# Performance work log

Measured on AMD Instinct MI355X. Metric: run time of the kernel, lower is better.

## Reference

```python
import jax, jax.numpy as jnp
import numpy as np

B, S, T, D = 8, 8, 256, 256          # batch, series, time_steps, input_dim
H, DK = 8, 64                         # attn_heads, attn_dim
HD = H * DK                           # 512
L = 2                                 # attn_layers
F = 256                               # mlp_dim
R = 512                               # resolution
M = 128                               # number of mid-points sampled this step
EPS = 1e-5


def setup_inputs() -> dict:
    key = jax.random.key(0)
    ks = iter(jax.random.split(key, 64))

    def rn(shape, scale=0.05):
        return scale * jax.random.normal(next(ks), shape, dtype=jnp.float32)

    inp = {
        'encoded': jax.random.normal(next(ks), (B, S, T, D), dtype=jnp.float32),
        'true_u': jax.random.uniform(next(ks), (B, S, T), dtype=jnp.float32),
        'mid_idx': jnp.sort(jax.random.randint(next(ks), (M,), 0, T)),
        'left_idx': jax.random.randint(next(ks), (M,), 0, T),
        'right_idx': jax.random.randint(next(ks), (M,), 0, T),
        'i': 3,
        # dimension_shift
        'ds_W': rn((D, HD)), 'ds_b': jnp.zeros((HD,), jnp.float32),
        # per-layer, per-head key-creator MLPs (stacked): (D+1) -> F -> F -> DK
        'kW1': rn((L, H, D + 1, F)), 'kb1': jnp.zeros((L, H, F), jnp.float32),
        'kW2': rn((L, H, F, F)),     'kb2': jnp.zeros((L, H, F), jnp.float32),
        'kW3': rn((L, H, F, DK)),    'kb3': jnp.zeros((L, H, DK), jnp.float32),
        # value-creator MLPs
        'vW1': rn((L, H, D + 1, F)), 'vb1': jnp.zeros((L, H, F), jnp.float32),
        'vW2': rn((L, H, F, F)),     'vb2': jnp.zeros((L, H, F), jnp.float32),
        'vW3': rn((L, H, F, DK)),    'vb3': jnp.zeros((L, H, DK), jnp.float32),
        # attention / feed-forward layer norms
        'ln1_g': jnp.ones((L, HD), jnp.float32), 'ln1_b': jnp.zeros((L, HD), jnp.float32),
        'ln2_g': jnp.ones((L, HD), jnp.float32), 'ln2_b': jnp.zeros((L, HD), jnp.float32),
        # feed-forwards
        'ffW1': rn((L, HD, HD)), 'ffb1': jnp.zeros((L, HD), jnp.float32),
        'ffW2': rn((L, HD, HD)), 'ffb2': jnp.zeros((L, HD), jnp.float32),
        # dist_extractors MLP: HD -> F -> F -> R
        'deW1': rn((HD, F)), 'deb1': jnp.zeros((F,), jnp.float32),
        'deW2': rn((F, F)),  'deb2': jnp.zeros((F,), jnp.float32),
        'deW3': rn((F, R)),  'deb3': jnp.zeros((R,), jnp.float32),
    }
    return inp


def _mlp_heads(x, W1, b1, W2, b2, W3, b3):
    # x: [B,S,T,D+1]; weights: [L,H,...] -> out [L,B,S,T,H,DK]
    h = jax.nn.relu(jnp.einsum('bstc,lhcf->lbsthf', x, W1) + b1[:, None, None, None])
    h = jax.nn.relu(jnp.einsum('lbsthf,lhfg->lbsthg', h, W2) + b2[:, None, None, None])
    return jnp.einsum('lbsthg,lhgd->lbsthd', h, W3) + b3[:, None, None, None]


def _ln(x, g, b):
    mu = jnp.mean(x, axis=-1, keepdims=True)
    var = jnp.mean(jnp.square(x - mu), axis=-1, keepdims=True)
    return (x - mu) * jax.lax.rsqrt(var + EPS) * g + b


def reference(encoded, true_u, mid_idx, left_idx, right_idx, i,
              ds_W, ds_b,
              kW1, kb1, kW2, kb2, kW3, kb3,
              vW1, vb1, vW2, vb2, vW3, vb3,
              ln1_g, ln1_b, ln2_g, ln2_b,
              ffW1, ffb1, ffW2, ffb2,
              deW1, deb1, deW2, deb2, deW3, deb3):
    # merged_input = cat([encoded, true_u[..., None]])  -> [B,S,T,D+1]
    merged = jnp.concatenate([encoded, true_u[..., None]], axis=-1)

    keys = _mlp_heads(merged, kW1, kb1, kW2, kb2, kW3, kb3)   # [L,B,S,T,H,DK]
    values = _mlp_heads(merged, vW1, vb1, vW2, vb2, vW3, vb3)  # [L,B,S,T,H,DK]

    srange = jnp.arange(S)
    # n=1 neighbor: time index = loop counter m for series < i, else right[m]
    # (faithful to keys_hist[:, :i, mid:mid+1] in the original)
    idx1 = jnp.where(srange[None, :] < i, jnp.arange(M)[:, None], right_idx[:, None])  # [M,S]

    def gather_neighbors(kv):  # kv: [L,B,S,T,H,DK] -> [L,B,M,S,2,H,DK]
        n0 = jnp.transpose(kv[:, :, :, left_idx], (0, 1, 3, 2, 4, 5))  # [L,B,M,S,H,DK]
        n1 = kv[:, :, srange[None, :], idx1]                            # [L,B,M,S,H,DK]
        return jnp.stack([n0, n1], axis=4)

    nk = gather_neighbors(keys)
    nv = gather_neighbors(values)

    pred = encoded[:, i, mid_idx]                  # [B,M,D]
    att_value = pred @ ds_W + ds_b                 # [B,M,HD]

    scale = DK ** (-0.5)
    for l in range(L):
        avh = att_value.reshape(B, M, H, DK)
        prod = jnp.einsum('bmhd,bmsnhd->bmhsn', avh, nk[l]) * scale
        w = jax.nn.softmax(prod, axis=-1)          # softmax over n only, as in source
        att = jnp.einsum('bmhsn,bmsnhd->bmhd', w, nv[l]).reshape(B, M, HD)
        x = _ln(att_value + att, ln1_g[l], ln1_b[l])
        ff = jax.nn.relu(x @ ffW1[l] + ffb1[l]) @ ffW2[l] + ffb2[l]
        att_value = _ln(x + ff, ln2_g[l], ln2_b[l])

    h = jax.nn.relu(att_value @ deW1 + deb1)
    h = jax.nn.relu(h @ deW2 + deb2)
    logits = h @ deW3 + deb3                       # [B,M,R]
    return logits
```

## Files before the change

kernel.cpp:

```cpp
#include <hip/hip_runtime.h>
#include <hip/hip_bf16.h>

#define NB 8
#define NS 8
#define NT 256
#define ND 256
#define NH 8
#define NDK 64
#define NHD 512
#define NL 2
#define NF 256
#define NR 512
#define NM 128
#define NTOK 16384
#define NROW 1024

typedef __attribute__((ext_vector_type(8))) short short8;
typedef __attribute__((ext_vector_type(4))) float f32x4;

__device__ __forceinline__ unsigned short f2bf(float x) {
    unsigned u = __builtin_bit_cast(unsigned, x);
    unsigned r = (u + 0x7fffu + ((u >> 16) & 1u)) >> 16;
    return (unsigned short)r;
}
__device__ __forceinline__ float bf2f(unsigned short x) {
    return __builtin_bit_cast(float, ((unsigned)x) << 16);
}
__device__ __forceinline__ float wred(float v) {
#pragma unroll
    for (int o = 32; o > 0; o >>= 1) v += __shfl_xor(v, o, 64);
    return v;
}

__global__ __launch_bounds__(256) void prep_all(
    const float* __restrict__ enc,
    const float* __restrict__ kW1, const float* __restrict__ kW2, const float* __restrict__ kW3,
    const float* __restrict__ vW1, const float* __restrict__ vW2, const float* __restrict__ vW3,
    const float* __restrict__ dsW, const float* __restrict__ ffW1,
    const float* __restrict__ ffW2, const float* __restrict__ deW1,
    const float* __restrict__ deW2, const float* __restrict__ deW3,
    unsigned short* __restrict__ XF, unsigned short* __restrict__ WP,
    float* __restrict__ W1L, unsigned short* __restrict__ WG) {
    __shared__ float T[32][257];
    int bid = blockIdx.x, tid = threadIdx.x;
    if (bid < 512) {
        int t0 = bid * 32;
        const float* src = enc + (size_t)t0 * 256;
#pragma unroll
        for (int it = 0; it < 8; ++it) {
            int f4 = it * 256 + tid;
            int row = f4 >> 6, c = (f4 & 63) * 4;
            float4 v = *(const float4*)(src + row * 256 + c);
            T[row][c] = v.x; T[row][c + 1] = v.y; T[row][c + 2] = v.z; T[row][c + 3] = v.w;
        }
        __syncthreads();
        int tile = t0 >> 7, g = (t0 >> 6) & 1, nt0 = (t0 >> 4) & 3;
#pragma unroll
        for (int i = 0; i < 32; i += 8) {
            int o = tid * 32 + i;
            int lane = (o >> 3) & 63, ntp = (o >> 9) & 1, kc = o >> 10;
            int id = lane & 15, quad = lane >> 4;
            __align__(16) unsigned short p[8];
#pragma unroll
            for (int j = 0; j < 8; ++j) p[j] = f2bf(T[ntp * 16 + id][kc * 32 + quad * 8 + j]);
            size_t dsto = ((size_t)((((tile * 8 + kc) * 2 + g) * 4 + (nt0 + ntp)) * 64 + lane)) * 8;
            *(uint4*)(XF + dsto) = *(uint4*)p;
        }
    } else if (bid < 1280) {
        int lb = bid - 512;
        int combo = lb / 24, r = lb % 24;
        int st = r >> 3, kc = r & 7;
        int kvv = combo >> 4, l = (combo >> 3) & 1, h = combo & 7;
        unsigned short* dstc = WP + (size_t)combo * 147456;
        if (st < 2) {
            const float* W = (st == 0) ? (kvv ? vW1 : kW1) : (kvv ? vW2 : kW2);
            int rows = (st == 0) ? 257 : 256;
            const float* src = W + ((size_t)(l * 8 + h) * rows + kc * 32) * 256;
#pragma unroll
            for (int it = 0; it < 8; ++it) {
                int f4 = it * 256 + tid;
                int row = f4 >> 6, c = (f4 & 63) * 4;
                float4 v = *(const float4*)(src + (size_t)row * 256 + c);
                T[row][c] = v.x; T[row][c + 1] = v.y; T[row][c + 2] = v.z; T[row][c + 3] = v.w;
            }
            __syncthreads();
            unsigned short* dst = dstc + st * 65536 + kc * 8192;
#pragma unroll
            for (int i = 0; i < 32; i += 8) {
                int o = tid * 32 + i;
                int lane = (o >> 3) & 63, ftile = o >> 9;
                int id = lane & 15, quad = lane >> 4;
                __align__(16) unsigned short p[8];
#pragma unroll
                for (int j = 0; j < 8; ++j) p[j] = f2bf(T[quad * 8 + j][ftile * 16 + id]);
                *(uint4*)(dst + o) = *(uint4*)p;
            }
            if (st == 0 && kc == 0) {
                const float* hw = (kvv ? vW1 : kW1) + (size_t)(l * 8 + h) * 257 * 256;
                W1L[combo * 256 + tid] = hw[65536 + tid];
            }
        } else {
            const float* src = (kvv ? vW3 : kW3) + ((size_t)(l * 8 + h) * 256 + kc * 32) * 64;
#pragma unroll
            for (int it = 0; it < 2; ++it) {
                int f4 = it * 256 + tid;
                int row = f4 >> 4, c = (f4 & 15) * 4;
                float4 v = *(const float4*)(src + (size_t)row * 64 + c);
                T[row][c] = v.x; T[row][c + 1] = v.y; T[row][c + 2] = v.z; T[row][c + 3] = v.w;
            }
            __syncthreads();
            unsigned short* dst = dstc + 131072 + kc * 2048;
            int o = tid * 8;
            int lane = tid & 63, ftile = tid >> 6;
            int id = lane & 15, quad = lane >> 4;
            __align__(16) unsigned short p[8];
#pragma unroll
            for (int j = 0; j < 8; ++j) p[j] = f2bf(T[quad * 8 + j][ftile * 16 + id]);
            *(uint4*)(dst + o) = *(uint4*)p;
        }
    } else {
        int lb0 = bid - 1280;
        const float* src; int N, kc, ng; size_t base;
        if (lb0 < 32)       { int lb = lb0;       src = dsW;           N = 512; base = 0;       kc = lb >> 2; ng = lb & 3; }
        else if (lb0 < 96)  { int lb = lb0 - 32;  src = ffW1;          N = 512; base = 131072;  kc = lb >> 2; ng = lb & 3; }
        else if (lb0 < 160) { int lb = lb0 - 96;  src = ffW1 + 262144; N = 512; base = 393216;  kc = lb >> 2; ng = lb & 3; }
        else if (lb0 < 224) { int lb = lb0 - 160; src = ffW2;          N = 512; base = 655360;  kc = lb >> 2; ng = lb & 3; }
        else if (lb0 < 288) { int lb = lb0 - 224; src = ffW2 + 262144; N = 512; base = 917504;  kc = lb >> 2; ng = lb & 3; }
        else if (lb0 < 320) { int lb = lb0 - 288; src = deW1;          N = 256; base = 1179648; kc = lb >> 1; ng = lb & 1; }
        else if (lb0 < 336) { int lb = lb0 - 320; src = deW2;          N = 256; base = 1310720; kc = lb >> 1; ng = lb & 1; }
        else                { int lb = lb0 - 336; src = deW3;          N = 512; base = 1376256; kc = lb >> 2; ng = lb & 3; }
        int NTl = N >> 4;
        const float* s = src + (size_t)(kc * 32) * N + ng * 128;
#pragma unroll
        for (int it = 0; it < 4; ++it) {
            int f4 = it * 256 + tid;
            int row = f4 >> 5, c = (f4 & 31) * 4;
            float4 v = *(const float4*)(s + (size_t)row * N + c);
            T[row][c] = v.x; T[row][c + 1] = v.y; T[row][c + 2] = v.z; T[row][c + 3] = v.w;
        }
        __syncthreads();
        unsigned short* d = WG + base + (size_t)(kc * NTl + ng * 8) * 512;
#pragma unroll
        for (int i = 0; i < 16; i += 8) {
            int o = tid * 16 + i;
            int lane = (o >> 3) & 63, ntl = o >> 9;
            int id = lane & 15, quad = lane >> 4;
            __align__(16) unsigned short p[8];
#pragma unroll
            for (int j = 0; j < 8; ++j) p[j] = f2bf(T[quad * 8 + j][ntl * 16 + id]);
            *(uint4*)(d + o) = *(uint4*)p;
        }
    }
}

__global__ __launch_bounds__(256, 4) void heads_mlp(
    const float* __restrict__ tu, const unsigned short* __restrict__ XF,
    const unsigned short* __restrict__ WP, const float* __restrict__ W1L,
    const float* __restrict__ kb1, const float* __restrict__ kb2, const float* __restrict__ kb3,
    const float* __restrict__ vb1, const float* __restrict__ vb2, const float* __restrict__ vb3,
    unsigned short* __restrict__ KV) {
    __shared__ __align__(16) unsigned short smem[16896];

    const int tid = threadIdx.x;
    const int w2 = tid >> 6, lane = tid & 63, id = lane & 15, quad = lane >> 4;
    const int combo = blockIdx.x & 31, t64 = blockIdx.x >> 5;
    const int kvv = combo >> 4, l = (combo >> 3) & 1, h = combo & 7;
    const int r0 = t64 * 64;
    const int tile128 = t64 >> 1, g = t64 & 1;
    const unsigned short* WF1 = WP + (size_t)combo * 147456;
    const unsigned short* WF2 = WF1 + 65536;
    const unsigned short* WF3 = WF1 + 131072;
    const float* b1 = (kvv ? vb1 : kb1) + (l * 8 + h) * 256;
    const float* b2 = (kvv ? vb2 : kb2) + (l * 8 + h) * 256;
    const float* b3 = (kvv ? vb3 : kb3) + (l * 8 + h) * 64;

    short8 afb[2][4];
#pragma unroll
    for (int ft = 0; ft < 4; ++ft) {
        afb[0][ft] = *(const short8*)(WF1 + (size_t)((w2 * 4 + ft) * 64 + lane) * 8);
        afb[1][ft] = *(const short8*)(WF1 + (size_t)((16 + w2 * 4 + ft) * 64 + lane) * 8);
    }
    {
        const uint4* s = (const uint4*)(XF + (size_t)tile128 * 32768 + g * 2048);
        uint4* d = (uint4*)smem;
#pragma unroll
        for (int kc = 0; kc < 8; ++kc) d[kc * 256 + tid] = s[kc * 512 + tid];
    }
    __syncthreads();

    f32x4 acc[4][4];
#pragma unroll
    for (int i = 0; i < 4; ++i)
#pragma unroll
        for (int j = 0; j < 4; ++j) acc[i][j] = (f32x4){0.f, 0.f, 0.f, 0.f};

    {
#pragma unroll
        for (int kc = 0; kc < 8; ++kc) {
            short8 tn[4];
            if (kc + 2 < 8) {
#pragma unroll
                for (int ft = 0; ft < 4; ++ft)
                    tn[ft] = *(const short8*)(WF1 + (size_t)(((kc + 2) * 16 + w2 * 4 + ft) * 64 + lane) * 8);
            }
            short8 bf[4];
#pragma unroll
            for (int nt = 0; nt < 4; ++nt)
                bf[nt] = *(const short8*)(smem + (size_t)(kc * 4 + nt) * 512 + lane * 8);
#pragma unroll
            for (int ft = 0; ft < 4; ++ft)
#pragma unroll
                for (int nt = 0; nt < 4; ++nt)
                    acc[ft][nt] = __builtin_amdgcn_mfma_f32_16x16x32_bf16(afb[kc & 1][ft], bf[nt], acc[ft][nt], 0, 0, 0);
            if (kc + 2 < 8) {
#pragma unroll
                for (int ft = 0; ft < 4; ++ft) afb[kc & 1][ft] = tn[ft];
            }
        }
    }
    __syncthreads();
    {
        float ur[4];
#pragma unroll
        for (int nt = 0; nt < 4; ++nt) ur[nt] = tu[r0 + nt * 16 + id];
#pragma unroll
        for (int ft = 0; ft < 4; ++ft) {
            int fb = w2 * 64 + ft * 16 + quad * 4;
            float4 bb = *(const float4*)(b1 + fb);
            float4 wl = *(const float4*)(W1L + combo * 256 + fb);
            const float* bbp = (const float*)&bb;
            const float* wlp = (const float*)&wl;
#pragma unroll
            for (int nt = 0; nt < 4; ++nt) {
                unsigned short p[4];
#pragma unroll
                for (int r = 0; r < 4; ++r) {
                    float v = acc[ft][nt][r] + bbp[r] + ur[nt] * wlp[r];
                    p[r] = f2bf(fmaxf(v, 0.f));
                }
                uint2 pk;
                pk.x = (unsigned)p[0] | ((unsigned)p[1] << 16);
                pk.y = (unsigned)p[2] | ((unsigned)p[3] << 16);
                *(uint2*)(smem + (size_t)(nt * 16 + id) * 264 + fb) = pk;
            }
        }
    }
    __syncthreads();

#pragma unroll
    for (int i = 0; i < 4; ++i)
#pragma unroll
        for (int j = 0; j < 4; ++j) acc[i][j] = (f32x4){0.f, 0.f, 0.f, 0.f};
    {
#pragma unroll
        for (int ft = 0; ft < 4; ++ft) {
            afb[0][ft] = *(const short8*)(WF2 + (size_t)((w2 * 4 + ft) * 64 + lane) * 8);
            afb[1][ft] = *(const short8*)(WF2 + (size_t)((16 + w2 * 4 + ft) * 64 + lane) * 8);
        }
#pragma unroll
        for (int kc = 0; kc < 8; ++kc) {
            short8 tn[4];
            if (kc + 2 < 8) {
#pragma unroll
                for (int ft = 0; ft < 4; ++ft)
                    tn[ft] = *(const short8*)(WF2 + (size_t)(((kc + 2) * 16 + w2 * 4 + ft) * 64 + lane) * 8);
            }
            short8 bf[4];
#pragma unroll
            for (int nt = 0; nt < 4; ++nt)
                bf[nt] = *(const short8*)(smem + (size_t)(nt * 16 + id) * 264 + kc * 32 + quad * 8);
#pragma unroll
            for (int ft = 0; ft < 4; ++ft)
#pragma unroll
                for (int nt = 0; nt < 4; ++nt)
                    acc[ft][nt] = __builtin_amdgcn_mfma_f32_16x16x32_bf16(afb[kc & 1][ft], bf[nt], acc[ft][nt], 0, 0, 0);
            if (kc + 2 < 8) {
#pragma unroll
                for (int ft = 0; ft < 4; ++ft) afb[kc & 1][ft] = tn[ft];
            }
        }
    }
    __syncthreads();
#pragma unroll
    for (int ft = 0; ft < 4; ++ft) {
        int fb = w2 * 64 + ft * 16 + quad * 4;
        float4 bb = *(const float4*)(b2 + fb);
        const float* bbp = (const float*)&bb;
#pragma unroll
        for (int nt = 0; nt < 4; ++nt) {
            unsigned short p[4];
#pragma unroll
            for (int r = 0; r < 4; ++r)
                p[r] = f2bf(fmaxf(acc[ft][nt][r] + bbp[r], 0.f));
            uint2 pk;
            pk.x = (unsigned)p[0] | ((unsigned)p[1] << 16);
            pk.y = (unsigned)p[2] | ((unsigned)p[3] << 16);
            *(uint2*)(smem + (size_t)(nt * 16 + id) * 264 + fb) = pk;
        }
    }
    __syncthreads();

    f32x4 a3[4];
#pragma unroll
    for (int i = 0; i < 4; ++i) a3[i] = (f32x4){0.f, 0.f, 0.f, 0.f};
    {
        short8 af3[4], af3n[4];
#pragma unroll
        for (int ft = 0; ft < 4; ++ft)
            af3[ft] = *(const short8*)(WF3 + (size_t)(ft * 64 + lane) * 8);
#pragma unroll
        for (int kc = 0; kc < 8; ++kc) {
            if (kc < 7) {
#pragma unroll
                for (int ft = 0; ft < 4; ++ft)
                    af3n[ft] = *(const short8*)(WF3 + (size_t)(((kc + 1) * 4 + ft) * 64 + lane) * 8);
            }
            short8 b3f = *(const short8*)(smem + (size_t)(w2 * 16 + id) * 264 + kc * 32 + quad * 8);
#pragma unroll
            for (int ft = 0; ft < 4; ++ft)
                a3[ft] = __builtin_amdgcn_mfma_f32_16x16x32_bf16(af3[ft], b3f, a3[ft], 0, 0, 0);
#pragma unroll
            for (int ft = 0; ft < 4; ++ft) af3[ft] = af3n[ft];
        }
    }
    __syncthreads();
    {
        int tl = w2 * 16 + id;
#pragma unroll
        for (int ft = 0; ft < 4; ++ft) {
            int dk0 = ft * 16 + quad * 4;
            float4 bb = *(const float4*)(b3 + dk0);
            const float* bbp = (const float*)&bb;
            unsigned short p[4];
#pragma unroll
            for (int r = 0; r < 4; ++r) p[r] = f2bf(a3[ft][r] + bbp[r]);
            uint2 pk;
            pk.x = (unsigned)p[0] | ((unsigned)p[1] << 16);
            pk.y = (unsigned)p[2] | ((unsigned)p[3] << 16);
            *(uint2*)(smem + (size_t)tl * 72 + dk0) = pk;
        }
    }
    __syncthreads();
    {
#pragma unroll
        for (int it = 0; it < 2; ++it) {
            int tl = it * 32 + (tid >> 3), part = tid & 7;
            uint4 v = *(const uint4*)(smem + (size_t)tl * 72 + part * 8);
            size_t base = ((size_t)combo << 20) + (size_t)(r0 + tl) * 64 + part * 8;
            *(uint4*)(KV + base) = v;
        }
    }
}

__global__ __launch_bounds__(256) void gemm_ds(
    const float* __restrict__ enc, const int* __restrict__ mid,
    const int* __restrict__ ip, const unsigned short* __restrict__ WF,
    const float* __restrict__ bias, float* __restrict__ outf) {
    int tid = threadIdx.x, wv = tid >> 6, lane = tid & 63;
    int id = lane & 15, quad = lane >> 4;
    int ntile = blockIdx.x * 4 + wv;
    int n0 = ntile * 16, m0 = blockIdx.y * 32;
    int iv = ip[0];
    int r0 = m0 + id, r1 = m0 + 16 + id;
    const float* a0p = enc + (((size_t)((r0 >> 7) * 8 + iv)) * 256 + mid[r0 & 127]) * 256 + quad * 8;
    const float* a1p = enc + (((size_t)((r1 >> 7) * 8 + iv)) * 256 + mid[r1 & 127]) * 256 + quad * 8;
    f32x4 acc[2];
    acc[0] = (f32x4){0.f, 0.f, 0.f, 0.f};
    acc[1] = (f32x4){0.f, 0.f, 0.f, 0.f};
#pragma unroll
    for (int kc = 0; kc < 8; ++kc) {
        short8 bw = *(const short8*)(WF + (size_t)((kc * 32 + ntile) * 64 + lane) * 8);
        float4 u0 = *(const float4*)(a0p + kc * 32);
        float4 u1 = *(const float4*)(a0p + kc * 32 + 4);
        float4 w0 = *(const float4*)(a1p + kc * 32);
        float4 w1 = *(const float4*)(a1p + kc * 32 + 4);
        short8 a0, a1;
        a0[0] = (short)f2bf(u0.x); a0[1] = (short)f2bf(u0.y); a0[2] = (short)f2bf(u0.z); a0[3] = (short)f2bf(u0.w);
        a0[4] = (short)f2bf(u1.x); a0[5] = (short)f2bf(u1.y); a0[6] = (short)f2bf(u1.z); a0[7] = (short)f2bf(u1.w);
        a1[0] = (short)f2bf(w0.x); a1[1] = (short)f2bf(w0.y); a1[2] = (short)f2bf(w0.z); a1[3] = (short)f2bf(w0.w);
        a1[4] = (short)f2bf(w1.x); a1[5] = (short)f2bf(w1.y); a1[6] = (short)f2bf(w1.z); a1[7] = (short)f2bf(w1.w);
        acc[0] = __builtin_amdgcn_mfma_f32_16x16x32_bf16(a0, bw, acc[0], 0, 0, 0);
        acc[1] = __builtin_amdgcn_mfma_f32_16x16x32_bf16(a1, bw, acc[1], 0, 0, 0);
    }
    float bv = bias[n0 + id];
#pragma unroll
    for (int mt = 0; mt < 2; ++mt) {
#pragma unroll
        for (int r = 0; r < 4; ++r) {
            int row = m0 + mt * 16 + quad * 4 + r;
            outf[(size_t)row * 512 + n0 + id] = acc[mt][r] + bv;
        }
    }
}

__global__ __launch_bounds__(256) void gemm_bf16(
    const unsigned short* __restrict__ A, const unsigned short* __restrict__ WF,
    const float* __restrict__ bias, const float* __restrict__ res,
    float* __restrict__ outf, unsigned short* __restrict__ outb,
    int K, int N, int relu) {
    int tid = threadIdx.x, wv = tid >> 6, lane = tid & 63;
    int id = lane & 15, quad = lane >> 4;
    int ntile = blockIdx.x * 4 + wv;
    int n0 = ntile * 16, m0 = blockIdx.y * 32;
    int NTl = N >> 4, KC = K >> 5;
    f32x4 acc[2];
    acc[0] = (f32x4){0.f, 0.f, 0.f, 0.f};
    acc[1] = (f32x4){0.f, 0.f, 0.f, 0.f};
    short8 bw = *(const short8*)(WF + (size_t)(ntile * 64 + lane) * 8);
    short8 a0 = *(const short8*)(A + (size_t)(m0 + id) * K + quad * 8);
    short8 a1 = *(const short8*)(A + (size_t)(m0 + 16 + id) * K + quad * 8);
    for (int kc = 0; kc < KC; ++kc) {
        short8 bwn, a0n, a1n;
        if (kc + 1 < KC) {
            bwn = *(const short8*)(WF + (size_t)(((kc + 1) * NTl + ntile) * 64 + lane) * 8);
            a0n = *(const short8*)(A + (size_t)(m0 + id) * K + (kc + 1) * 32 + quad * 8);
            a1n = *(const short8*)(A + (size_t)(m0 + 16 + id) * K + (kc + 1) * 32 + quad * 8);
        }
        acc[0] = __builtin_amdgcn_mfma_f32_16x16x32_bf16(a0, bw, acc[0], 0, 0, 0);
        acc[1] = __builtin_amdgcn_mfma_f32_16x16x32_bf16(a1, bw, acc[1], 0, 0, 0);
        bw = bwn; a0 = a0n; a1 = a1n;
    }
    float bv = bias[n0 + id];
#pragma unroll
    for (int mt = 0; mt < 2; ++mt) {
#pragma unroll
        for (int r = 0; r < 4; ++r) {
            int row = m0 + mt * 16 + quad * 4 + r;
            int n = n0 + id;
            float v = acc[mt][r] + bv;
            if (res) v += res[(size_t)row * N + n];
            if (relu) v = fmaxf(v, 0.f);
            if (outf) outf[(size_t)row * N + n] = v;
            if (outb) outb[(size_t)row * N + n] = f2bf(v);
        }
    }
}

__global__ __launch_bounds__(256) void attn_ln(
    const float* __restrict__ attv, const unsigned short* __restrict__ KV,
    const int* __restrict__ left, const int* __restrict__ right,
    const int* __restrict__ ip,
    const float* __restrict__ g, const float* __restrict__ bb,
    float* __restrict__ xout, unsigned short* __restrict__ xoutb, int l) {
    int tid = threadIdx.x, wv = tid >> 6, lane = tid & 63;
    int gid = blockIdx.x * 4 + wv;
    int b = gid >> 7, m = gid & 127;
    int iv = ip[0];
    int lt = left[m], rt = right[m];
    int h = lane >> 3, d8 = lane & 7;
    const unsigned short* kb = KV + ((size_t)(l * 8 + h) << 20);
    const unsigned short* vb = KV + ((size_t)(16 + l * 8 + h) << 20);
    float av8[8], att8[8];
    {
        const float* avp = attv + (size_t)gid * 512 + lane * 8;
        float4 u0 = *(const float4*)(avp);
        float4 u1 = *(const float4*)(avp + 4);
        av8[0] = u0.x; av8[1] = u0.y; av8[2] = u0.z; av8[3] = u0.w;
        av8[4] = u1.x; av8[5] = u1.y; av8[6] = u1.z; av8[7] = u1.w;
    }
#pragma unroll
    for (int j = 0; j < 8; ++j) att8[j] = 0.f;
#pragma unroll 2
    for (int s = 0; s < 8; ++s) {
        int t1 = (s < iv) ? m : rt;
        size_t o0 = (size_t)((b * 8 + s) * 256 + lt) * 64 + d8 * 8;
        size_t o1 = (size_t)((b * 8 + s) * 256 + t1) * 64 + d8 * 8;
        uint4 k0u = *(const uint4*)(kb + o0);
        uint4 k1u = *(const uint4*)(kb + o1);
        uint4 v0u = *(const uint4*)(vb + o0);
        uint4 v1u = *(const uint4*)(vb + o1);
        const unsigned short* k0 = (const unsigned short*)&k0u;
        const unsigned short* k1 = (const unsigned short*)&k1u;
        const unsigned short* v0 = (const unsigned short*)&v0u;
        const unsigned short* v1 = (const unsigned short*)&v1u;
        float p0 = 0.f, p1 = 0.f;
#pragma unroll
        for (int j = 0; j < 8; ++j) {
            p0 += av8[j] * bf2f(k0[j]);
            p1 += av8[j] * bf2f(k1[j]);
        }
#pragma unroll
        for (int o = 1; o < 8; o <<= 1) {
            p0 += __shfl_xor(p0, o, 64);
            p1 += __shfl_xor(p1, o, 64);
        }
        p0 *= 0.125f; p1 *= 0.125f;
        float mx = fmaxf(p0, p1);
        float e0 = __expf(p0 - mx), e1 = __expf(p1 - mx);
        float inv = 1.f / (e0 + e1);
        float w0 = e0 * inv, w1 = e1 * inv;
#pragma unroll
        for (int j = 0; j < 8; ++j)
            att8[j] += w0 * bf2f(v0[j]) + w1 * bf2f(v1[j]);
    }
    float x8[8], sum = 0.f;
#pragma unroll
    for (int j = 0; j < 8; ++j) { x8[j] = av8[j] + att8[j]; sum += x8[j]; }
    float mu = wred(sum) * (1.f / 512.f);
    float s2 = 0.f;
#pragma unroll
    for (int j = 0; j < 8; ++j) { float d = x8[j] - mu; s2 += d * d; }
    float rs = rsqrtf(wred(s2) * (1.f / 512.f) + 1e-5f);
    {
        const float* gp = g + lane * 8;
        const float* bp = bb + lane * 8;
        float* of = xout + (size_t)gid * 512 + lane * 8;
        unsigned short* ob = xoutb + (size_t)gid * 512 + lane * 8;
        __align__(16) float vout[8];
        __align__(16) unsigned short pb[8];
#pragma unroll
        for (int j = 0; j < 8; ++j) {
            float v = (x8[j] - mu) * rs * gp[j] + bp[j];
            vout[j] = v; pb[j] = f2bf(v);
        }
        *(float4*)(of) = *(float4*)vout;
        *(float4*)(of + 4) = *(float4*)(vout + 4);
        *(uint4*)(ob) = *(uint4*)pb;
    }
}

__global__ __launch_bounds__(256) void ln_k(const float* __restrict__ in,
                                            const float* __restrict__ g,
                                            const float* __restrict__ bb,
                                            float* __restrict__ out,
                                            unsigned short* __restrict__ outb) {
    int tid = threadIdx.x, wv = tid >> 6, lane = tid & 63;
    int gid = blockIdx.x * 4 + wv;
    float x8[8], sum = 0.f;
    {
        const float* ip = in + (size_t)gid * 512 + lane * 8;
        float4 u0 = *(const float4*)(ip);
        float4 u1 = *(const float4*)(ip + 4);
        x8[0] = u0.x; x8[1] = u0.y; x8[2] = u0.z; x8[3] = u0.w;
        x8[4] = u1.x; x8[5] = u1.y; x8[6] = u1.z; x8[7] = u1.w;
    }
#pragma unroll
    for (int j = 0; j < 8; ++j) sum += x8[j];
    float mu = wred(sum) * (1.f / 512.f);
    float s2 = 0.f;
#pragma unroll
    for (int j = 0; j < 8; ++j) { float d = x8[j] - mu; s2 += d * d; }
    float rs = rsqrtf(wred(s2) * (1.f / 512.f) + 1e-5f);
    {
        const float* gp = g + lane * 8;
        const float* bp = bb + lane * 8;
        float* of = out + (size_t)gid * 512 + lane * 8;
        unsigned short* ob = outb + (size_t)gid * 512 + lane * 8;
        __align__(16) float vout[8];
        __align__(16) unsigned short pb[8];
#pragma unroll
        for (int j = 0; j < 8; ++j) {
            float v = (x8[j] - mu) * rs * gp[j] + bp[j];
            vout[j] = v; pb[j] = f2bf(v);
        }
        *(float4*)(of) = *(float4*)vout;
        *(float4*)(of + 4) = *(float4*)(vout + 4);
        *(uint4*)(ob) = *(uint4*)pb;
    }
}

extern "C" void kernel_launch(void* const* d_in, const int* in_sizes, int n_in,
                              void* d_out, int out_size, void* d_ws, size_t ws_size,
                              hipStream_t stream) {
    const float* encoded = (const float*)d_in[0];
    const float* true_u  = (const float*)d_in[1];
    const int* mid_idx   = (const int*)d_in[2];
    const int* left_idx  = (const int*)d_in[3];
    const int* right_idx = (const int*)d_in[4];
    const int* ip        = (const int*)d_in[5];
    const float* ds_W = (const float*)d_in[6];
    const float* ds_b = (const float*)d_in[7];
    const float* kW1 = (const float*)d_in[8];
    const float* kb1 = (const float*)d_in[9];
    const float* kW2 = (const float*)d_in[10];
    const float* kb2 = (const float*)d_in[11];
    const float* kW3 = (const float*)d_in[12];
    const float* kb3 = (const float*)d_in[13];
    const float* vW1 = (const float*)d_in[14];
    const float* vb1 = (const float*)d_in[15];
    const float* vW2 = (const float*)d_in[16];
    const float* vb2 = (const float*)d_in[17];
    const float* vW3 = (const float*)d_in[18];
    const float* vb3 = (const float*)d_in[19];
    const float* ln1_g = (const float*)d_in[20];
    const float* ln1_b = (const float*)d_in[21];
    const float* ln2_g = (const float*)d_in[22];
    const float* ln2_b = (const float*)d_in[23];
    const float* ffW1 = (const float*)d_in[24];
    const float* ffb1 = (const float*)d_in[25];
    const float* ffW2 = (const float*)d_in[26];
    const float* ffb2 = (const float*)d_in[27];
    const float* deW1 = (const float*)d_in[28];
    const float* deb1 = (const float*)d_in[29];
    const float* deW2 = (const float*)d_in[30];
    const float* deb2 = (const float*)d_in[31];
    const float* deW3 = (const float*)d_in[32];
    const float* deb3 = (const float*)d_in[33];

    char* ws = (char*)d_ws;
    unsigned short* XF    = (unsigned short*)(ws + 0);
    unsigned short* WP    = (unsigned short*)(ws + 8388608);
    float* W1L            = (float*)(ws + 17825792);
    unsigned short* KV    = (unsigned short*)(ws + 17858560);
    unsigned short* WG    = (unsigned short*)(ws + 84967424);
    float* ATTV           = (float*)(ws + 87982080);
    float* XBUF           = (float*)(ws + 90079232);
    float* YBUF           = (float*)(ws + 92176384);
    unsigned short* ATTVB = (unsigned short*)(ws + 94273536);
    unsigned short* XBUFB = (unsigned short*)(ws + 95322112);
    unsigned short* FBUFB = (unsigned short*)(ws + 96370688);
    unsigned short* DE1B = XBUFB;
    unsigned short* DE2B = FBUFB;

    unsigned short* WGds    = WG + 0;
    unsigned short* WGff1_0 = WG + 131072;
    unsigned short* WGff1_1 = WG + 393216;
    unsigned short* WGff2_0 = WG + 655360;
    unsigned short* WGff2_1 = WG + 917504;
    unsigned short* WGde1   = WG + 1179648;
    unsigned short* WGde2   = WG + 1310720;
    unsigned short* WGde3   = WG + 1376256;

    prep_all<<<1648, 256, 0, stream>>>(encoded, kW1, kW2, kW3, vW1, vW2, vW3,
                                       ds_W, ffW1, ffW2, deW1, deW2, deW3,
                                       XF, WP, W1L, WG);
    heads_mlp<<<8192, 256, 0, stream>>>(true_u, XF, WP, W1L, kb1, kb2, kb3,
                                        vb1, vb2, vb3, KV);
    gemm_ds<<<dim3(8, 32), 256, 0, stream>>>(encoded, mid_idx, ip, WGds, ds_b, ATTV);
    for (int l = 0; l < 2; ++l) {
        attn_ln<<<256, 256, 0, stream>>>(ATTV, KV, left_idx, right_idx, ip,
                                         ln1_g + l * 512, ln1_b + l * 512,
                                         XBUF, XBUFB, l);
        gemm_bf16<<<dim3(8, 32), 256, 0, stream>>>(XBUFB, (l ? WGff1_1 : WGff1_0),
                                                   ffb1 + l * 512, nullptr,
                                                   nullptr, FBUFB, 512, 512, 1);
        gemm_bf16<<<dim3(8, 32), 256, 0, stream>>>(FBUFB, (l ? WGff2_1 : WGff2_0),
                                                   ffb2 + l * 512, XBUF,
                                                   YBUF, nullptr, 512, 512, 0);
        ln_k<<<256, 256, 0, stream>>>(YBUF, ln2_g + l * 512, ln2_b + l * 512, ATTV, ATTVB);
    }
    gemm_bf16<<<dim3(4, 32), 256, 0, stream>>>(ATTVB, WGde1, deb1, nullptr,
                                               nullptr, DE1B, 512, 256, 1);
    gemm_bf16<<<dim3(4, 32), 256, 0, stream>>>(DE1B, WGde2, deb2, nullptr,
                                               nullptr, DE2B, 256, 256, 1);
    gemm_bf16<<<dim3(8, 32), 256, 0, stream>>>(DE2B, WGde3, deb3, nullptr,
                                               (float*)d_out, nullptr, 256, 512, 0);
}
```

Baseline: 440.1 us.

## Fuse tail kernels into one persistent kernel with atomic grid barriers

Replaces the chain of twelve small tail launches (ds projection, attention+LN, FF GEMMs, LN, distribution MLP) with one 256-block persistent kernel. Stages are separated by software grid barriers built on atomic counters, which are zeroed in prep_all. This removes per-launch overhead and the idle gaps between small kernels. The barriers assume all 256 blocks are resident at once and add spin-wait cost at each stage boundary.

Result: slower. 581.2 us (+32.1%).

```diff
diff --git a/kernel.cpp b/kernel.cpp
--- a/kernel.cpp
+++ b/kernel.cpp
@@ -32,6 +32,17 @@
     return v;
 }
 
+__device__ __forceinline__ void gridbar(unsigned* c) {
+    __syncthreads();
+    if (threadIdx.x == 0) {
+        __hip_atomic_fetch_add(c, 1u, __ATOMIC_RELEASE, __HIP_MEMORY_SCOPE_AGENT);
+        while (__hip_atomic_load(c, __ATOMIC_RELAXED, __HIP_MEMORY_SCOPE_AGENT) < 256u)
+            __builtin_amdgcn_s_sleep(16);
+        (void)__hip_atomic_load(c, __ATOMIC_ACQUIRE, __HIP_MEMORY_SCOPE_AGENT);
+    }
+    __syncthreads();
+}
+
 __global__ __launch_bounds__(256) void prep_all(
     const float* __restrict__ enc,
     const float* __restrict__ kW1, const float* __restrict__ kW2, const float* __restrict__ kW3,
@@ -40,9 +51,11 @@
     const float* __restrict__ ffW2, const float* __restrict__ deW1,
     const float* __restrict__ deW2, const float* __restrict__ deW3,
     unsigned short* __restrict__ XF, unsigned short* __restrict__ WP,
-    float* __restrict__ W1L, unsigned short* __restrict__ WG) {
+    float* __restrict__ W1L, unsigned short* __restrict__ WG,
+    unsigned* __restrict__ BAR) {
     __shared__ float T[32][257];
     int bid = blockIdx.x, tid = threadIdx.x;
+    if (bid == 0 && tid < 16) BAR[tid] = 0;
     if (bid < 512) {
         int t0 = bid * 32;
         const float* src = enc + (size_t)t0 * 256;
@@ -352,60 +365,18 @@
     }
 }
 
-__global__ __launch_bounds__(256) void gemm_ds(
-    const float* __restrict__ enc, const int* __restrict__ mid,
-    const int* __restrict__ ip, const unsigned short* __restrict__ WF,
-    const float* __restrict__ bias, float* __restrict__ outf) {
-    int tid = threadIdx.x, wv = tid >> 6, lane = tid & 63;
-    int id = lane & 15, quad = lane >> 4;
-    int ntile = blockIdx.x * 4 + wv;
-    int n0 = ntile * 16, m0 = blockIdx.y * 32;
-    int iv = ip[0];
-    int r0 = m0 + id, r1 = m0 + 16 + id;
-    const float* a0p = enc + (((size_t)((r0 >> 7) * 8 + iv)) * 256 + mid[r0 & 127]) * 256 + quad * 8;
-    const float* a1p = enc + (((size_t)((r1 >> 7) * 8 + iv)) * 256 + mid[r1 & 127]) * 256 + quad * 8;
-    f32x4 acc[2];
-    acc[0] = (f32x4){0.f, 0.f, 0.f, 0.f};
-    acc[1] = (f32x4){0.f, 0.f, 0.f, 0.f};
-#pragma unroll
-    for (int kc = 0; kc < 8; ++kc) {
-        short8 bw = *(const short8*)(WF + (size_t)((kc * 32 + ntile) * 64 + lane) * 8);
-        float4 u0 = *(const float4*)(a0p + kc * 32);
-        float4 u1 = *(const float4*)(a0p + kc * 32 + 4);
-        float4 w0 = *(const float4*)(a1p + kc * 32);
-        float4 w1 = *(const float4*)(a1p + kc * 32 + 4);
-        short8 a0, a1;
-        a0[0] = (short)f2bf(u0.x); a0[1] = (short)f2bf(u0.y); a0[2] = (short)f2bf(u0.z); a0[3] = (short)f2bf(u0.w);
-        a0[4] = (short)f2bf(u1.x); a0[5] = (short)f2bf(u1.y); a0[6] = (short)f2bf(u1.z); a0[7] = (short)f2bf(u1.w);
-        a1[0] = (short)f2bf(w0.x); a1[1] = (short)f2bf(w0.y); a1[2] = (short)f2bf(w0.z); a1[3] = (short)f2bf(w0.w);
-        a1[4] = (short)f2bf(w1.x); a1[5] = (short)f2bf(w1.y); a1[6] = (short)f2bf(w1.z); a1[7] = (short)f2bf(w1.w);
-        acc[0] = __builtin_amdgcn_mfma_f32_16x16x32_bf16(a0, bw, acc[0], 0, 0, 0);
-        acc[1] = __builtin_amdgcn_mfma_f32_16x16x32_bf16(a1, bw, acc[1], 0, 0, 0);
-    }
-    float bv = bias[n0 + id];
-#pragma unroll
-    for (int mt = 0; mt < 2; ++mt) {
-#pragma unroll
-        for (int r = 0; r < 4; ++r) {
-            int row = m0 + mt * 16 + quad * 4 + r;
-            outf[(size_t)row * 512 + n0 + id] = acc[mt][r] + bv;
-        }
-    }
-}
-
-__global__ __launch_bounds__(256) void gemm_bf16(
+__device__ __forceinline__ void gemm_stage(
     const unsigned short* __restrict__ A, const unsigned short* __restrict__ WF,
     const float* __restrict__ bias, const float* __restrict__ res,
     float* __restrict__ outf, unsigned short* __restrict__ outb,
-    int K, int N, int relu) {
+    int K, int N, int relu, int bx, int by) {
     int tid = threadIdx.x, wv = tid >> 6, lane = tid & 63;
     int id = lane & 15, quad = lane >> 4;
-    int ntile = blockIdx.x * 4 + wv;
-    int n0 = ntile * 16, m0 = blockIdx.y * 32;
+    int ntile = bx * 4 + wv;
+    int n0 = ntile * 16, m0 = by * 32;
     int NTl = N >> 4, KC = K >> 5;
-    f32x4 acc[2];
-    acc[0] = (f32x4){0.f, 0.f, 0.f, 0.f};
-    acc[1] = (f32x4){0.f, 0.f, 0.f, 0.f};
+    f32x4 acc0 = (f32x4){0.f, 0.f, 0.f, 0.f};
+    f32x4 acc1 = (f32x4){0.f, 0.f, 0.f, 0.f};
     short8 bw = *(const short8*)(WF + (size_t)(ntile * 64 + lane) * 8);
     short8 a0 = *(const short8*)(A + (size_t)(m0 + id) * K + quad * 8);
     short8 a1 = *(const short8*)(A + (size_t)(m0 + 16 + id) * K + quad * 8);
@@ -416,18 +387,19 @@
             a0n = *(const short8*)(A + (size_t)(m0 + id) * K + (kc + 1) * 32 + quad * 8);
             a1n = *(const short8*)(A + (size_t)(m0 + 16 + id) * K + (kc + 1) * 32 + quad * 8);
         }
-        acc[0] = __builtin_amdgcn_mfma_f32_16x16x32_bf16(a0, bw, acc[0], 0, 0, 0);
-        acc[1] = __builtin_amdgcn_mfma_f32_16x16x32_bf16(a1, bw, acc[1], 0, 0, 0);
+        acc0 = __builtin_amdgcn_mfma_f32_16x16x32_bf16(a0, bw, acc0, 0, 0, 0);
+        acc1 = __builtin_amdgcn_mfma_f32_16x16x32_bf16(a1, bw, acc1, 0, 0, 0);
         bw = bwn; a0 = a0n; a1 = a1n;
     }
     float bv = bias[n0 + id];
 #pragma unroll
     for (int mt = 0; mt < 2; ++mt) {
+        f32x4 av = mt ? acc1 : acc0;
 #pragma unroll
         for (int r = 0; r < 4; ++r) {
             int row = m0 + mt * 16 + quad * 4 + r;
             int n = n0 + id;
-            float v = acc[mt][r] + bv;
+            float v = av[r] + bv;
             if (res) v += res[(size_t)row * N + n];
             if (relu) v = fmaxf(v, 0.f);
             if (outf) outf[(size_t)row * N + n] = v;
@@ -436,127 +408,196 @@
     }
 }
 
-__global__ __launch_bounds__(256) void attn_ln(
-    const float* __restrict__ attv, const unsigned short* __restrict__ KV,
+__global__ __launch_bounds__(256) void tail_fused(
+    const float* __restrict__ enc, const int* __restrict__ mid,
     const int* __restrict__ left, const int* __restrict__ right,
     const int* __restrict__ ip,
-    const float* __restrict__ g, const float* __restrict__ bb,
-    float* __restrict__ xout, unsigned short* __restrict__ xoutb, int l) {
-    int tid = threadIdx.x, wv = tid >> 6, lane = tid & 63;
-    int gid = blockIdx.x * 4 + wv;
-    int b = gid >> 7, m = gid & 127;
-    int iv = ip[0];
-    int lt = left[m], rt = right[m];
-    int h = lane >> 3, d8 = lane & 7;
-    const unsigned short* kb = KV + ((size_t)(l * 8 + h) << 20);
-    const unsigned short* vb = KV + ((size_t)(16 + l * 8 + h) << 20);
-    float av8[8], att8[8];
-    {
-        const float* avp = attv + (size_t)gid * 512 + lane * 8;
-        float4 u0 = *(const float4*)(avp);
-        float4 u1 = *(const float4*)(avp + 4);
-        av8[0] = u0.x; av8[1] = u0.y; av8[2] = u0.z; av8[3] = u0.w;
-        av8[4] = u1.x; av8[5] = u1.y; av8[6] = u1.z; av8[7] = u1.w;
-    }
-#pragma unroll
-    for (int j = 0; j < 8; ++j) att8[j] = 0.f;
+    const unsigned short* __restrict__ KV, const unsigned short* __restrict__ WG,
+    const float* __restrict__ ds_b,
+    const float* __restrict__ ln1_g, const float* __restrict__ ln1_b,
+    const float* __restrict__ ln2_g, const float* __restrict__ ln2_b,
+    const float* __restrict__ ffb1, const float* __restrict__ ffb2,
+    const float* __restrict__ deb1, const float* __restrict__ deb2,
+    const float* __restrict__ deb3,
+    float* __restrict__ ATTV, float* __restrict__ XBUF, float* __restrict__ YBUF,
+    unsigned short* __restrict__ ATTVB, unsigned short* __restrict__ XBUFB,
+    unsigned short* __restrict__ FBUFB,
+    float* __restrict__ out, unsigned* __restrict__ BAR) {
+    const int bid = blockIdx.x;
+    const int tid = threadIdx.x;
+    const int wv = tid >> 6, lane = tid & 63, id = lane & 15, quad = lane >> 4;
+    const int iv = ip[0];
+
+    {
+        int bx = bid & 7, by = bid >> 3;
+        int ntile = bx * 4 + wv;
+        int n0 = ntile * 16, m0 = by * 32;
+        int r0 = m0 + id, r1 = m0 + 16 + id;
+        const float* a0p = enc + (((size_t)((r0 >> 7) * 8 + iv)) * 256 + mid[r0 & 127]) * 256 + quad * 8;
+        const float* a1p = enc + (((size_t)((r1 >> 7) * 8 + iv)) * 256 + mid[r1 & 127]) * 256 + quad * 8;
+        f32x4 acc0 = (f32x4){0.f, 0.f, 0.f, 0.f};
+        f32x4 acc1 = (f32x4){0.f, 0.f, 0.f, 0.f};
+#pragma unroll
+        for (int kc = 0; kc < 8; ++kc) {
+            short8 bw = *(const short8*)(WG + (size_t)((kc * 32 + ntile) * 64 + lane) * 8);
+            float4 u0 = *(const float4*)(a0p + kc * 32);
+            float4 u1 = *(const float4*)(a0p + kc * 32 + 4);
+            float4 w0 = *(const float4*)(a1p + kc * 32);
+            float4 w1 = *(const float4*)(a1p + kc * 32 + 4);
+            short8 a0, a1;
+            a0[0] = (short)f2bf(u0.x); a0[1] = (short)f2bf(u0.y); a0[2] = (short)f2bf(u0.z); a0[3] = (short)f2bf(u0.w);
+            a0[4] = (short)f2bf(u1.x); a0[5] = (short)f2bf(u1.y); a0[6] = (short)f2bf(u1.z); a0[7] = (short)f2bf(u1.w);
+            a1[0] = (short)f2bf(w0.x); a1[1] = (short)f2bf(w0.y); a1[2] = (short)f2bf(w0.z); a1[3] = (short)f2bf(w0.w);
+            a1[4] = (short)f2bf(w1.x); a1[5] = (short)f2bf(w1.y); a1[6] = (short)f2bf(w1.z); a1[7] = (short)f2bf(w1.w);
+            acc0 = __builtin_amdgcn_mfma_f32_16x16x32_bf16(a0, bw, acc0, 0, 0, 0);
+            acc1 = __builtin_amdgcn_mfma_f32_16x16x32_bf16(a1, bw, acc1, 0, 0, 0);
+        }
+        float bv = ds_b[n0 + id];
+#pragma unroll
+        for (int mt = 0; mt < 2; ++mt) {
+            f32x4 av = mt ? acc1 : acc0;
+#pragma unroll
+            for (int r = 0; r < 4; ++r) {
+                int row = m0 + mt * 16 + quad * 4 + r;
+                ATTV[(size_t)row * 512 + n0 + id] = av[r] + bv;
+            }
+        }
+    }
+    gridbar(BAR + 0);
+
+    for (int l = 0; l < 2; ++l) {
+        {
+            int gid = bid * 4 + wv;
+            int b = gid >> 7, m = gid & 127;
+            int lt = left[m], rt = right[m];
+            int h = lane >> 3, d8 = lane & 7;
+            const unsigned short* kb = KV + ((size_t)(l * 8 + h) << 20);
+            const unsigned short* vb = KV + ((size_t)(16 + l * 8 + h) << 20);
+            const float* g1 = ln1_g + l * 512;
+            const float* bb1 = ln1_b + l * 512;
+            float av8[8], att8[8];
+            {
+                const float* avp = ATTV + (size_t)gid * 512 + lane * 8;
+                float4 u0 = *(const float4*)(avp);
+                float4 u1 = *(const float4*)(avp + 4);
+                av8[0] = u0.x; av8[1] = u0.y; av8[2] = u0.z; av8[3] = u0.w;
+                av8[4] = u1.x; av8[5] = u1.y; av8[6] = u1.z; av8[7] = u1.w;
+            }
+#pragma unroll
+            for (int j = 0; j < 8; ++j) att8[j] = 0.f;
 #pragma unroll 2
-    for (int s = 0; s < 8; ++s) {
-        int t1 = (s < iv) ? m : rt;
-        size_t o0 = (size_t)((b * 8 + s) * 256 + lt) * 64 + d8 * 8;
-        size_t o1 = (size_t)((b * 8 + s) * 256 + t1) * 64 + d8 * 8;
-        uint4 k0u = *(const uint4*)(kb + o0);
-        uint4 k1u = *(const uint4*)(kb + o1);
-        uint4 v0u = *(const uint4*)(vb + o0);
-        uint4 v1u = *(const uint4*)(vb + o1);
-        const unsigned short* k0 = (const unsigned short*)&k0u;
-        const unsigned short* k1 = (const unsigned short*)&k1u;
-        const unsigned short* v0 = (const unsigned short*)&v0u;
-        const unsigned short* v1 = (const unsigned short*)&v1u;
-        float p0 = 0.f, p1 = 0.f;
-#pragma unroll
-        for (int j = 0; j < 8; ++j) {
-            p0 += av8[j] * bf2f(k0[j]);
-            p1 += av8[j] * bf2f(k1[j]);
-        }
-#pragma unroll
-        for (int o = 1; o < 8; o <<= 1) {
-            p0 += __shfl_xor(p0, o, 64);
-            p1 += __shfl_xor(p1, o, 64);
-        }
-        p0 *= 0.125f; p1 *= 0.125f;
-        float mx = fmaxf(p0, p1);
-        float e0 = __expf(p0 - mx), e1 = __expf(p1 - mx);
-        float inv = 1.f / (e0 + e1);
-        float w0 = e0 * inv, w1 = e1 * inv;
-#pragma unroll
-        for (int j = 0; j < 8; ++j)
-            att8[j] += w0 * bf2f(v0[j]) + w1 * bf2f(v1[j]);
-    }
-    float x8[8], sum = 0.f;
-#pragma unroll
-    for (int j = 0; j < 8; ++j) { x8[j] = av8[j] + att8[j]; sum += x8[j]; }
-    float mu = wred(sum) * (1.f / 512.f);
-    float s2 = 0.f;
-#pragma unroll
-    for (int j = 0; j < 8; ++j) { float d = x8[j] - mu; s2 += d * d; }
-    float rs = rsqrtf(wred(s2) * (1.f / 512.f) + 1e-5f);
-    {
-        const float* gp = g + lane * 8;
-        const float* bp = bb + lane * 8;
-        float* of = xout + (size_t)gid * 512 + lane * 8;
-        unsigned short* ob = xoutb + (size_t)gid * 512 + lane * 8;
-        __align__(16) float vout[8];
-        __align__(16) unsigned short pb[8];
-#pragma unroll
-        for (int j = 0; j < 8; ++j) {
-            float v = (x8[j] - mu) * rs * gp[j] + bp[j];
-            vout[j] = v; pb[j] = f2bf(v);
-        }
-        *(float4*)(of) = *(float4*)vout;
-        *(float4*)(of + 4) = *(float4*)(vout + 4);
-        *(uint4*)(ob) = *(uint4*)pb;
-    }
-}
-
-__global__ __launch_bounds__(256) void ln_k(const float* __restrict__ in,
-                                            const float* __restrict__ g,
-                                            const float* __restrict__ bb,
-                                            float* __restrict__ out,
-                                            unsigned short* __restrict__ outb) {
-    int tid = threadIdx.x, wv = tid >> 6, lane = tid & 63;
-    int gid = blockIdx.x * 4 + wv;
-    float x8[8], sum = 0.f;
-    {
-        const float* ip = in + (size_t)gid * 512 + lane * 8;
-        float4 u0 = *(const float4*)(ip);
-        float4 u1 = *(const float4*)(ip + 4);
-        x8[0] = u0.x; x8[1] = u0.y; x8[2] = u0.z; x8[3] = u0.w;
-        x8[4] = u1.x; x8[5] = u1.y; x8[6] = u1.z; x8[7] = u1.w;
-    }
-#pragma unroll
-    for (int j = 0; j < 8; ++j) sum += x8[j];
-    float mu = wred(sum) * (1.f / 512.f);
-    float s2 = 0.f;
-#pragma unroll
-    for (int j = 0; j < 8; ++j) { float d = x8[j] - mu; s2 += d * d; }
-    float rs = rsqrtf(wred(s2) * (1.f / 512.f) + 1e-5f);
-    {
-        const float* gp = g + lane * 8;
-        const float* bp = bb + lane * 8;
-        float* of = out + (size_t)gid * 512 + lane * 8;
-        unsigned short* ob = outb + (size_t)gid * 512 + lane * 8;
-        __align__(16) float vout[8];
-        __align__(16) unsigned short pb[8];
-#pragma unroll
-        for (int j = 0; j < 8; ++j) {
-            float v = (x8[j] - mu) * rs * gp[j] + bp[j];
-            vout[j] = v; pb[j] = f2bf(v);
-        }
-        *(float4*)(of) = *(float4*)vout;
-        *(float4*)(of + 4) = *(float4*)(vout + 4);
-        *(uint4*)(ob) = *(uint4*)pb;
-    }
+            for (int s = 0; s < 8; ++s) {
+                int t1 = (s < iv) ? m : rt;
+                size_t o0 = (size_t)((b * 8 + s) * 256 + lt) * 64 + d8 * 8;
+                size_t o1 = (size_t)((b * 8 + s) * 256 + t1) * 64 + d8 * 8;
+                uint4 k0u = *(const uint4*)(kb + o0);
+                uint4 k1u = *(const uint4*)(kb + o1);
+                uint4 v0u = *(const uint4*)(vb + o0);
+                uint4 v1u = *(const uint4*)(vb + o1);
+                const unsigned short* k0 = (const unsigned short*)&k0u;
+                const unsigned short* k1 = (const unsigned short*)&k1u;
+                const unsigned short* v0 = (const unsigned short*)&v0u;
+                const unsigned short* v1 = (const unsigned short*)&v1u;
+                float p0 = 0.f, p1 = 0.f;
+#pragma unroll
+                for (int j = 0; j < 8; ++j) {
+                    p0 += av8[j] * bf2f(k0[j]);
+                    p1 += av8[j] * bf2f(k1[j]);
+                }
+#pragma unroll
+                for (int o = 1; o < 8; o <<= 1) {
+                    p0 += __shfl_xor(p0, o, 64);
+                    p1 += __shfl_xor(p1, o, 64);
+                }
+                p0 *= 0.125f; p1 *= 0.125f;
+                float mx = fmaxf(p0, p1);
+                float e0 = __expf(p0 - mx), e1 = __expf(p1 - mx);
+                float inv = 1.f / (e0 + e1);
+                float w0 = e0 * inv, w1 = e1 * inv;
+#pragma unroll
+                for (int j = 0; j < 8; ++j)
+                    att8[j] += w0 * bf2f(v0[j]) + w1 * bf2f(v1[j]);
+            }
+            float x8[8], sum = 0.f;
+#pragma unroll
+            for (int j = 0; j < 8; ++j) { x8[j] = av8[j] + att8[j]; sum += x8[j]; }
+            float mu = wred(sum) * (1.f / 512.f);
+            float s2 = 0.f;
+#pragma unroll
+            for (int j = 0; j < 8; ++j) { float d = x8[j] - mu; s2 += d * d; }
+            float rs = rsqrtf(wred(s2) * (1.f / 512.f) + 1e-5f);
+            const float* gp = g1 + lane * 8;
+            const float* bp = bb1 + lane * 8;
+            float* of = XBUF + (size_t)gid * 512 + lane * 8;
+            unsigned short* ob = XBUFB + (size_t)gid * 512 + lane * 8;
+            __align__(16) float vout[8];
+            __align__(16) unsigned short pb[8];
+#pragma unroll
+            for (int j = 0; j < 8; ++j) {
+                float v = (x8[j] - mu) * rs * gp[j] + bp[j];
+                vout[j] = v; pb[j] = f2bf(v);
+            }
+            *(float4*)(of) = *(float4*)vout;
+            *(float4*)(of + 4) = *(float4*)(vout + 4);
+            *(uint4*)(ob) = *(uint4*)pb;
+        }
+        gridbar(BAR + 1 + l * 4);
+
+        gemm_stage(XBUFB, WG + 131072 + (size_t)l * 262144, ffb1 + l * 512,
+                   nullptr, nullptr, FBUFB, 512, 512, 1, bid & 7, bid >> 3);
+        gridbar(BAR + 2 + l * 4);
+
+        gemm_stage(FBUFB, WG + 655360 + (size_t)l * 262144, ffb2 + l * 512,
+                   XBUF, YBUF, nullptr, 512, 512, 0, bid & 7, bid >> 3);
+        gridbar(BAR + 3 + l * 4);
+
+        {
+            int gid = bid * 4 + wv;
+            const float* g2 = ln2_g + l * 512;
+            const float* bb2 = ln2_b + l * 512;
+            float x8[8], sum = 0.f;
+            {
+                const float* ipt = YBUF + (size_t)gid * 512 + lane * 8;
+                float4 u0 = *(const float4*)(ipt);
+                float4 u1 = *(const float4*)(ipt + 4);
+                x8[0] = u0.x; x8[1] = u0.y; x8[2] = u0.z; x8[3] = u0.w;
+                x8[4] = u1.x; x8[5] = u1.y; x8[6] = u1.z; x8[7] = u1.w;
+            }
+#pragma unroll
+            for (int j = 0; j < 8; ++j) sum += x8[j];
+            float mu = wred(sum) * (1.f / 512.f);
+            float s2 = 0.f;
+#pragma unroll
+            for (int j = 0; j < 8; ++j) { float d = x8[j] - mu; s2 += d * d; }
+            float rs = rsqrtf(wred(s2) * (1.f / 512.f) + 1e-5f);
+            const float* gp = g2 + lane * 8;
+            const float* bp = bb2 + lane * 8;
+            float* of = ATTV + (size_t)gid * 512 + lane * 8;
+            unsigned short* ob = ATTVB + (size_t)gid * 512 + lane * 8;
+            __align__(16) float vout[8];
+            __align__(16) unsigned short pb[8];
+#pragma unroll
+            for (int j = 0; j < 8; ++j) {
+                float v = (x8[j] - mu) * rs * gp[j] + bp[j];
+                vout[j] = v; pb[j] = f2bf(v);
+            }
+            *(float4*)(of) = *(float4*)vout;
+            *(float4*)(of + 4) = *(float4*)(vout + 4);
+            *(uint4*)(ob) = *(uint4*)pb;
+        }
+        gridbar(BAR + 4 + l * 4);
+    }
+
+    if (bid < 128)
+        gemm_stage(ATTVB, WG + 1179648, deb1, nullptr, nullptr, XBUFB,
+                   512, 256, 1, bid & 3, bid >> 2);
+    gridbar(BAR + 9);
+    if (bid < 128)
+        gemm_stage(XBUFB, WG + 1310720, deb2, nullptr, nullptr, FBUFB,
+                   256, 256, 1, bid & 3, bid >> 2);
+    gridbar(BAR + 10);
+    gemm_stage(FBUFB, WG + 1376256, deb3, nullptr, out, nullptr,
+               256, 512, 0, bid & 7, bid >> 3);
 }
 
 extern "C" void kernel_launch(void* const* d_in, const int* in_sizes, int n_in,
@@ -609,40 +650,16 @@
     unsigned short* ATTVB = (unsigned short*)(ws + 94273536);
     unsigned short* XBUFB = (unsigned short*)(ws + 95322112);
     unsigned short* FBUFB = (unsigned short*)(ws + 96370688);
-    unsigned short* DE1B = XBUFB;
-    unsigned short* DE2B = FBUFB;
-
-    unsigned short* WGds    = WG + 0;
-    unsigned short* WGff1_0 = WG + 131072;
-    unsigned short* WGff1_1 = WG + 393216;
-    unsigned short* WGff2_0 = WG + 655360;
-    unsigned short* WGff2_1 = WG + 917504;
-    unsigned short* WGde1   = WG + 1179648;
-    unsigned short* WGde2   = WG + 1310720;
-    unsigned short* WGde3   = WG + 1376256;
+    unsigned* BAR         = (unsigned*)(ws + 97419264);
 
     prep_all<<<1648, 256, 0, stream>>>(encoded, kW1, kW2, kW3, vW1, vW2, vW3,
                                        ds_W, ffW1, ffW2, deW1, deW2, deW3,
-                                       XF, WP, W1L, WG);
+                                       XF, WP, W1L, WG, BAR);
     heads_mlp<<<8192, 256, 0, stream>>>(true_u, XF, WP, W1L, kb1, kb2, kb3,
                                         vb1, vb2, vb3, KV);
-    gemm_ds<<<dim3(8, 32), 256, 0, stream>>>(encoded, mid_idx, ip, WGds, ds_b, ATTV);
-    for (int l = 0; l < 2; ++l) {
-        attn_ln<<<256, 256, 0, stream>>>(ATTV, KV, left_idx, right_idx, ip,
-                                         ln1_g + l * 512, ln1_b + l * 512,
-                                         XBUF, XBUFB, l);
-        gemm_bf16<<<dim3(8, 32), 256, 0, stream>>>(XBUFB, (l ? WGff1_1 : WGff1_0),
-                                                   ffb1 + l * 512, nullptr,
-                                                   nullptr, FBUFB, 512, 512, 1);
-        gemm_bf16<<<dim3(8, 32), 256, 0, stream>>>(FBUFB, (l ? WGff2_1 : WGff2_0),
-                                                   ffb2 + l * 512, XBUF,
-                                                   YBUF, nullptr, 512, 512, 0);
-        ln_k<<<256, 256, 0, stream>>>(YBUF, ln2_g + l * 512, ln2_b + l * 512, ATTV, ATTVB);
-    }
-    gemm_bf16<<<dim3(4, 32), 256, 0, stream>>>(ATTVB, WGde1, deb1, nullptr,
-                                               nullptr, DE1B, 512, 256, 1);
-    gemm_bf16<<<dim3(4, 32), 256, 0, stream>>>(DE1B, WGde2, deb2, nullptr,
-                                               nullptr, DE2B, 256, 256, 1);
-    gemm_bf16<<<dim3(8, 32), 256, 0, stream>>>(DE2B, WGde3, deb3, nullptr,
-                                               (float*)d_out, nullptr, 256, 512, 0);
-}
+    tail_fused<<<256, 256, 0, stream>>>(encoded, mid_idx, left_idx, right_idx, ip,
+                                        KV, WG, ds_b, ln1_g, ln1_b, ln2_g, ln2_b,
+                                        ffb1, ffb2, deb1, deb2, deb3,
+                                        ATTV, XBUF, YBUF, ATTVB, XBUFB, FBUFB,
+                                        (float*)d_out, BAR);
+}
```
